# Kernel tuning notes

Hardware: AMD Instinct MI355X
Metric: run time of the kernel (lower is better)

The kernel has to match this reference:

```python
import jax, jax.numpy as jnp
from jax import lax
import numpy as np

D_MODEL = 128
N_HEADS = 8
N_POINTS = 8
MAX_MAG = 10.0
NEG_SLOPE = 0.1


def conv2d(x, w, b, pad):
    # x: (N, Cin, H, W), w: (Cout, Cin, kh, kw)
    y = lax.conv_general_dilated(x, w, (1, 1), [(pad, pad), (pad, pad)],
                                 dimension_numbers=('NCHW', 'OIHW', 'NCHW'))
    return y + b[None, :, None, None]


def leaky(x):
    return jnp.where(x >= 0, x, NEG_SLOPE * x)


def bilinear_sample(img, grid):
    # img: (B, C, H, W); grid: (B, P, H, W, 2) in [-1, 1] (x, y)
    # Matches torch F.grid_sample(mode='bilinear', padding_mode='zeros', align_corners=False)
    B, C, H, W = img.shape
    x = ((grid[..., 0] + 1.0) * W - 1.0) * 0.5
    y = ((grid[..., 1] + 1.0) * H - 1.0) * 0.5
    x0 = jnp.floor(x)
    y0 = jnp.floor(y)
    wx1 = x - x0
    wy1 = y - y0

    def one(img_b, x0b, y0b, wx1b, wy1b):
        def gather(xi, yi):
            valid = (xi >= 0) & (xi < W) & (yi >= 0) & (yi < H)
            xc = jnp.clip(xi, 0, W - 1).astype(jnp.int32)
            yc = jnp.clip(yi, 0, H - 1).astype(jnp.int32)
            v = img_b[:, yc, xc]  # (C, P, H, W)
            return v * valid
        wx0b = 1.0 - wx1b
        wy0b = 1.0 - wy1b
        v00 = gather(x0b, y0b)
        v01 = gather(x0b + 1, y0b)
        v10 = gather(x0b, y0b + 1)
        v11 = gather(x0b + 1, y0b + 1)
        return (v00 * (wx0b * wy0b) + v01 * (wx1b * wy0b)
                + v10 * (wx0b * wy1b) + v11 * (wx1b * wy1b))

    return jax.vmap(one)(img, x0, y0, wx1, wy1)  # (B, C, P, H, W)


def ss_deform_attn(value, loc):
    # value: (N, nh, d, H, W); loc: (N, nh, P, H, W, 2) in normalized [0,1] coords
    N, nh, d, H, W = value.shape
    P = loc.shape[2]
    v = value.reshape(N * nh, d, H, W)
    grids = (2.0 * loc - 1.0).reshape(N * nh, P, H, W, 2)
    sampled = bilinear_sample(v, grids)  # (N*nh, d, P, H, W)
    # per-location attention logits = <sampled_point, value_at_location>
    scores = jnp.einsum('ndphw,ndhw->nphw', sampled, v)
    aw = jax.nn.softmax(scores, axis=1)
    out = jnp.einsum('ndphw,nphw->ndhw', sampled, aw)
    return out.reshape(N, nh * d, H, W)


def _forward(query, value, reference_points, co_w1, co_b1, co_w2, co_b2,
             co_w3, co_b3, co_w4, co_b4, val_w, val_b, out_w, out_b):
    N, C, H, W = value.shape
    v = conv2d(value, val_w, val_b, 0)
    v = v.reshape(N, N_HEADS, D_MODEL // N_HEADS, H, W)
    o = leaky(conv2d(query, co_w1, co_b1, 1))
    o = leaky(conv2d(o, co_w2, co_b2, 1))
    o = leaky(conv2d(o, co_w3, co_b3, 1))
    o = conv2d(o, co_w4, co_b4, 1)
    o = MAX_MAG * jnp.tanh(o)
    offsets = o.reshape(N, N_HEADS, N_POINTS, H, W, 2)
    norm = jnp.array([W, H], dtype=o.dtype)  # (x, y) normalizer
    loc = reference_points[:, None, None, :, :, :] + offsets / norm
    out = ss_deform_attn(v, loc)
    return conv2d(out, out_w, out_b, 0)


def setup_inputs() -> dict:
    key = jax.random.key(0)
    ks = jax.random.split(key, 12)
    N, H, W = 4, 80, 80

    def w_init(k, shape):
        fan_in = shape[1] * shape[2] * shape[3]
        return jax.random.normal(k, shape, jnp.float32) / np.sqrt(fan_in)

    return {
        'query': jax.random.normal(ks[0], (N, 2 * D_MODEL, H, W), jnp.float32),
        'value': jax.random.normal(ks[1], (N, D_MODEL, H, W), jnp.float32),
        'reference_points': jax.random.uniform(ks[2], (N, H, W, 2), jnp.float32),
        'co_w1': w_init(ks[3], (D_MODEL, 2 * D_MODEL, 3, 3)),
        'co_b1': jnp.zeros((D_MODEL,), jnp.float32),
        'co_w2': w_init(ks[4], (D_MODEL, D_MODEL, 3, 3)),
        'co_b2': jnp.zeros((D_MODEL,), jnp.float32),
        'co_w3': w_init(ks[5], (D_MODEL, D_MODEL, 3, 3)),
        'co_b3': jnp.zeros((D_MODEL,), jnp.float32),
        'co_w4': w_init(ks[6], (N_HEADS * N_POINTS * 2, D_MODEL, 3, 3)),
        'co_b4': jnp.zeros((N_HEADS * N_POINTS * 2,), jnp.float32),
        'val_w': w_init(ks[7], (D_MODEL, D_MODEL, 1, 1)),
        'val_b': jnp.zeros((D_MODEL,), jnp.float32),
        'out_w': w_init(ks[8], (D_MODEL, D_MODEL, 1, 1)),
        'out_b': jnp.zeros((D_MODEL,), jnp.float32),
    }


def reference(query, value, reference_points, co_w1, co_b1, co_w2, co_b2,
              co_w3, co_b3, co_w4, co_b4, val_w, val_b, out_w, out_b):
    return _forward(query, value, reference_points, co_w1, co_b1, co_w2, co_b2,
                    co_w3, co_b3, co_w4, co_b4, val_w, val_b, out_w, out_b)
```

## Files before the change

kernel.cpp:

```cpp
#include <hip/hip_runtime.h>
#include <math.h>

#define Hh 80
#define Ww 80
#define HW 6400
#define PS 6724
#define NB 4

typedef _Float16 half8 __attribute__((ext_vector_type(8)));
typedef _Float16 half4v __attribute__((ext_vector_type(4)));
typedef float f32x16 __attribute__((ext_vector_type(16)));

__device__ __forceinline__ void gload16(const _Float16* g, _Float16* l) {
    __builtin_amdgcn_global_load_lds(
        (const __attribute__((address_space(1))) void*)g,
        (__attribute__((address_space(3))) void*)l, 16, 0, 0);
}

#define WAITVM(N) asm volatile("s_waitcnt vmcnt(" #N ")" ::: "memory")
#define FENCE() asm volatile("" ::: "memory")

__device__ __forceinline__ void barrier_mem() {
    asm volatile("" ::: "memory");
    __builtin_amdgcn_s_barrier();
    asm volatile("" ::: "memory");
}

__device__ inline void wblob_one(const float* src, _Float16* dst, int CI, int d) {
    int NC = CI / 32;
    int j = d & 7;
    int l = (d >> 3) & 63;
    int h = (d >> 9) & 1;
    int rest = d >> 10;
    int tap = rest % 9;
    rest /= 9;
    int c = rest % NC;
    int CT = rest / NC;
    int co = CT * 32 + (l & 31);
    int ci = c * 32 + h * 16 + (l >> 5) * 8 + j;
    dst[d] = (_Float16)src[((size_t)co * CI + ci) * 9 + tap];
}

__device__ inline void wblob1x1_one(const float* src, _Float16* dst, int d) {
    int j = d & 7;
    int l = (d >> 3) & 63;
    int c = (d >> 9) & 7;
    int CT = d >> 12;
    int co = CT * 32 + (l & 31);
    int ci = c * 16 + (l >> 5) * 8 + j;
    dst[d] = (_Float16)src[co * 128 + ci];
}

__device__ inline int padsite(int p) {
    if (p < 82) return p;
    if (p < 164) return 81 * 82 + (p - 82);
    if (p < 244) return (p - 163) * 82;
    return (p - 243) * 82 + 81;
}

__global__ __launch_bounds__(256) void prep_all(
    const float* __restrict__ w1, const float* __restrict__ w2,
    const float* __restrict__ w3, const float* __restrict__ w4,
    const float* __restrict__ vw, const float* __restrict__ ow,
    _Float16* __restrict__ b1, _Float16* __restrict__ b2,
    _Float16* __restrict__ b3, _Float16* __restrict__ b4,
    _Float16* __restrict__ bv, _Float16* __restrict__ bo,
    int* __restrict__ qh_i, int* __restrict__ hA_i, int* __restrict__ hB_i,
    const float* __restrict__ query, const float* __restrict__ value,
    _Float16* __restrict__ q_h, _Float16* __restrict__ v_h) {
    __shared__ _Float16 T[64 * 264];
    const int blk = blockIdx.x;
    const int t = threadIdx.x;

    if (blk < 4304) {
        int idx = blk * 256 + t;
        if (idx < 294912) { wblob_one(w1, b1, 256, idx); return; }
        idx -= 294912;
        if (idx < 147456) { wblob_one(w2, b2, 128, idx); return; }
        idx -= 147456;
        if (idx < 147456) { wblob_one(w3, b3, 128, idx); return; }
        idx -= 147456;
        if (idx < 147456) { wblob_one(w4, b4, 128, idx); return; }
        idx -= 147456;
        if (idx < 16384) { wblob1x1_one(vw, bv, idx); return; }
        idx -= 16384;
        if (idx < 16384) { wblob1x1_one(ow, bo, idx); return; }
        idx -= 16384;
        if (idx < 165888) {
            int n = idx / 41472, rr = idx % 41472;
            int c = rr / 5184, r2 = rr % 5184;
            int p = r2 >> 4, k = r2 & 15;
            qh_i[((size_t)(n * 8 + c) * PS + padsite(p)) * 16 + k] = 0;
            return;
        }
        idx -= 165888;
        if (idx < 82944) {
            int n = idx / 20736, rr = idx % 20736;
            int c = rr / 5184, r2 = rr % 5184;
            int p = r2 >> 4, k = r2 & 15;
            hA_i[((size_t)(n * 4 + c) * PS + padsite(p)) * 16 + k] = 0;
            return;
        }
        idx -= 82944;
        if (idx < 82944) {
            int n = idx / 20736, rr = idx % 20736;
            int c = rr / 5184, r2 = rr % 5184;
            int p = r2 >> 4, k = r2 & 15;
            hB_i[((size_t)(n * 4 + c) * PS + padsite(p)) * 16 + k] = 0;
        }
        return;
    }

    if (blk < 4704) {
        const int b = blk - 4304;
        const int xcd = b & 7, n = xcd & 3, hi = xcd >> 2;
        const int s0 = hi * 3200 + (b >> 3) * 64;
        constexpr int CI = 256, ST = CI + 8;
        for (int idx = t; idx < 64 * CI; idx += 256) {
            int ci = idx >> 6, sl = idx & 63;
            T[sl * ST + ci] = (_Float16)query[((size_t)n * CI + ci) * HW + s0 + sl];
        }
        __syncthreads();
        for (int idx = t; idx < 64 * 32; idx += 256) {
            int q = idx & 31, sl = idx >> 5;
            int s = s0 + sl, yy = s / 80, xx = s % 80;
            int c = q >> 2, off = (q & 3) * 8;
            *(int4*)(q_h + ((size_t)(n * 8 + c) * PS + (yy + 1) * 82 + (xx + 1)) * 32 + off) =
                *(const int4*)(&T[sl * ST + q * 8]);
        }
        return;
    }

    {
        const int b = blk - 4704;
        const int xcd = b & 7, n = xcd & 3, hi = xcd >> 2;
        const int s0 = hi * 3200 + (b >> 3) * 64;
        constexpr int CI = 128, ST = CI + 8;
        for (int idx = t; idx < 64 * CI; idx += 256) {
            int ci = idx >> 6, sl = idx & 63;
            T[sl * ST + ci] = (_Float16)value[((size_t)n * CI + ci) * HW + s0 + sl];
        }
        __syncthreads();
        for (int idx = t; idx < 64 * 16; idx += 256) {
            int q = idx & 15, sl = idx >> 4;
            *(int4*)(v_h + ((size_t)n * HW + s0 + sl) * CI + q * 8) =
                *(const int4*)(&T[sl * ST + q * 8]);
        }
    }
}

template <int NCp, int ACT>
__device__ __forceinline__ void conv3x3_body(
    int b, const _Float16* __restrict__ in, const _Float16* __restrict__ wblob,
    const float* __restrict__ bias, void* __restrict__ outp) {
    constexpr int NS = NCp * 18;
    static_assert((NCp & 1) == 0, "pair loop needs even NCp");
    __shared__ _Float16 Bbuf[2][6 * 1024];

    const int xcd = b & 7, n = xcd & 3, hi = xcd >> 2;
    const int r = b >> 3;
    const int x0 = (r % 5) * 16, y0 = hi * 40 + (r / 5) * 4;
    const int t = threadIdx.x;
    const int w = t >> 6, l = t & 63;
    const int lane31 = l & 31, lhalf = l >> 5;
    const int lx = lane31 & 15, lyw = lane31 >> 4;
    const int si = l & 15, g8 = l >> 4;

    const _Float16* bplane0 = in + (size_t)(n * NCp) * PS * 32;
    const _Float16* wA = wblob + (size_t)w * NS * 512 + l * 8;

    f32x16 acc0 = {}, acc1 = {};
    half8 aA[6], aB[6];

    auto stageB = [&](const _Float16* plane, int par) {
#pragma unroll
        for (int j = 0; j < 3; ++j) {
            const int m = 3 * w + j, rr = m >> 1, sg = m & 1;
            gload16(plane + ((size_t)((y0 + rr) * 82 + x0 + sg * 16 + si)) * 32 + g8 * 8,
                    &Bbuf[par][rr * 1024 + sg * 512]);
        }
    };
    auto loadA6 = [&](half8 (&ar)[6], int grp) {
        const _Float16* asrc = wA + (size_t)grp * 6 * 512;
#pragma unroll
        for (int k2 = 0; k2 < 6; ++k2)
            ar[k2] = *(const half8*)(asrc + (size_t)k2 * 512);
    };
    auto compute6 = [&](int gi, const half8 (&ar)[6], const _Float16* bb) {
#pragma unroll
        for (int k = 0; k < 6; ++k) {
            const int u = gi * 6 + k;
            const int tap = u >> 1, h = u & 1;
            const int dy = tap / 3, dx = tap % 3;
            const int cx = lx + dx;
            const int boff = (cx >> 4) * 512 + (h * 2 + lhalf) * 128 + (cx & 15) * 8;
            half8 b0 = *(const half8*)&bb[(lyw + dy) * 1024 + boff];
            half8 b1 = *(const half8*)&bb[(lyw + 2 + dy) * 1024 + boff];
            acc0 = __builtin_amdgcn_mfma_f32_32x32x16_f16(ar[k], b0, acc0, 0, 0, 0);
            acc1 = __builtin_amdgcn_mfma_f32_32x32x16_f16(ar[k], b1, acc1, 0, 0, 0);
        }
    };

    stageB(bplane0, 0);
    loadA6(aA, 0);
    WAITVM(0);
    barrier_mem();

#pragma unroll 1
    for (int cp = 0; cp < NCp / 2; ++cp) {
        const int c0 = 2 * cp;
        const bool lastp = (cp == NCp / 2 - 1);
        const _Float16* plane1 = bplane0 + (size_t)(c0 + 1) * PS * 32;
        const _Float16* plane2 = bplane0 + (size_t)(c0 + 2) * PS * 32;
        loadA6(aB, c0 * 3 + 1);
        stageB(plane1, 1);
        FENCE();
        compute6(0, aA, Bbuf[0]);
        loadA6(aA, c0 * 3 + 2);
        FENCE();
        compute6(1, aB, Bbuf[0]);
        loadA6(aB, c0 * 3 + 3);
        FENCE();
        compute6(2, aA, Bbuf[0]);
        WAITVM(12);
        barrier_mem();
        loadA6(aA, c0 * 3 + 4);
        if (!lastp) stageB(plane2, 0);
        FENCE();
        compute6(0, aB, Bbuf[1]);
        loadA6(aB, c0 * 3 + 5);
        FENCE();
        compute6(1, aA, Bbuf[1]);
        if (!lastp) {
            loadA6(aA, c0 * 3 + 6);
            FENCE();
            compute6(2, aB, Bbuf[1]);
            WAITVM(12);
            barrier_mem();
        } else {
            FENCE();
            compute6(2, aB, Bbuf[1]);
        }
    }

    const int x = x0 + lx;
#pragma unroll
    for (int f = 0; f < 2; ++f) {
        const f32x16& acc = f ? acc1 : acc0;
        const int y = y0 + lyw + 2 * f;
#pragma unroll
        for (int q = 0; q < 4; ++q) {
            const int inner = 8 * q + 4 * lhalf;
            const int co0 = w * 32 + inner;
            float v[4];
#pragma unroll
            for (int i = 0; i < 4; ++i) {
                float vv = acc[q * 4 + i] + bias[co0 + i];
                if (ACT == 1) vv = (vv >= 0.f) ? vv : 0.1f * vv;
                else vv = 10.f * tanhf(vv);
                v[i] = vv;
            }
            if (ACT == 1) {
                half4v hv = {(_Float16)v[0], (_Float16)v[1], (_Float16)v[2], (_Float16)v[3]};
                *(half4v*)((_Float16*)outp +
                    ((size_t)(n * 4 + w) * PS + (y + 1) * 82 + (x + 1)) * 32 + inner) = hv;
            } else {
                float4 fv = {v[0], v[1], v[2], v[3]};
                *(float4*)((float*)outp + ((size_t)n * HW + y * 80 + x) * 128 + co0) = fv;
            }
        }
    }
}

template <int NCp, int ACT>
__global__ __launch_bounds__(256, 2) void conv3x3_mfma(
    const _Float16* __restrict__ in, const _Float16* __restrict__ wblob,
    const float* __restrict__ bias, void* __restrict__ outp) {
    conv3x3_body<NCp, ACT>(blockIdx.x, in, wblob, bias, outp);
}

template <int MODE>
__device__ __forceinline__ void conv1x1_body(
    int b, const _Float16* __restrict__ in, const _Float16* __restrict__ wblob,
    const float* __restrict__ bias, float* __restrict__ outp) {
    const int xcd = b & 7, n = xcd & 3, hi = xcd >> 2;
    const int r = b >> 3;
    const int coH = r & 1, strip = r >> 1;
    const int t = threadIdx.x;
    const int w = t >> 6, l = t & 63;
    const int lane31 = l & 31, lhalf = l >> 5;
    const int s = hi * 3200 + strip * 128 + w * 32 + lane31;

    const _Float16* pB = in + (size_t)(n * HW + s) * 128 + lhalf * 8;
    const _Float16* pA0 = wblob + (size_t)(coH * 2) * 8 * 512 + l * 8;
    const _Float16* pA1 = pA0 + 8 * 512;

    half8 bB[8], bA0[8], bA1[8];
#pragma unroll
    for (int c = 0; c < 8; ++c) {
        bB[c]  = *(const half8*)(pB + c * 16);
        bA0[c] = *(const half8*)(pA0 + (size_t)c * 512);
        bA1[c] = *(const half8*)(pA1 + (size_t)c * 512);
    }
    f32x16 acc0 = {}, acc1 = {};
#pragma unroll
    for (int c = 0; c < 8; ++c) {
        acc0 = __builtin_amdgcn_mfma_f32_32x32x16_f16(bA0[c], bB[c], acc0, 0, 0, 0);
        acc1 = __builtin_amdgcn_mfma_f32_32x32x16_f16(bA1[c], bB[c], acc1, 0, 0, 0);
    }

#pragma unroll
    for (int ct = 0; ct < 2; ++ct) {
        const f32x16& acc = ct ? acc1 : acc0;
#pragma unroll
        for (int q = 0; q < 4; ++q) {
            const int co0 = coH * 64 + ct * 32 + 8 * q + 4 * lhalf;
            if (MODE == 0) {
                const int hd = co0 >> 4, dd = co0 & 15;
                float4 fv = {acc[4 * q + 0] + bias[co0 + 0], acc[4 * q + 1] + bias[co0 + 1],
                             acc[4 * q + 2] + bias[co0 + 2], acc[4 * q + 3] + bias[co0 + 3]};
                *(float4*)&outp[((size_t)(n * 8 + hd) * HW + s) * 16 + dd] = fv;
            } else {
#pragma unroll
                for (int i = 0; i < 4; ++i)
                    outp[(size_t)(n * 128 + co0 + i) * HW + s] = acc[4 * q + i] + bias[co0 + i];
            }
        }
    }
}

template <int MODE>
__global__ __launch_bounds__(256) void conv1x1_mfma(
    const _Float16* __restrict__ in, const _Float16* __restrict__ wblob,
    const float* __restrict__ bias, float* __restrict__ outp) {
    conv1x1_body<MODE>(blockIdx.x, in, wblob, bias, outp);
}

__global__ __launch_bounds__(256, 2) void conv1_val_fused(
    const _Float16* __restrict__ q_h, const _Float16* __restrict__ wb1,
    const float* __restrict__ co_b1, void* __restrict__ hA,
    const _Float16* __restrict__ v_h, const _Float16* __restrict__ wbv,
    const float* __restrict__ val_b, float* __restrict__ v_s) {
    const int b = blockIdx.x;
    if (b < 400) {
        conv3x3_body<8, 1>(b, q_h, wb1, co_b1, hA);
    } else {
        conv1x1_body<0>(b - 400, v_h, wbv, val_b, v_s);
    }
}

__global__ __launch_bounds__(256, 4) void deform_attn_kernel(
    const float* __restrict__ v_s, const float* __restrict__ offs,
    const float* __restrict__ ref, _Float16* __restrict__ att) {
    const int slice = blockIdx.x;
    const int n = slice >> 3, hd = slice & 7;
    const int t = threadIdx.x;
    const int s = blockIdx.y * 32 + (t >> 3);
    const int sub = t & 7;
    const int d0 = (sub & 3) * 4;
    const int ph = sub >> 2;
    const int nb = n * 8 + hd;
    const float* vbase = v_s + (size_t)nb * (HW * 16) + d0;

    const float4 cv = *(const float4*)&v_s[((size_t)nb * HW + s) * 16 + d0];
    const float rx = ref[(size_t)(n * HW + s) * 2 + 0] * 80.f - 0.5f;
    const float ry = ref[(size_t)(n * HW + s) * 2 + 1] * 80.f - 0.5f;

    const int e = (s >= 3200) ? 1 : 0;
    const float* ob0 = offs + ((size_t)n * HW + (2 * s - e * HW)) * 128 + hd * 16 + e;

    float4 oxv0 = *(const float4*)(ob0 + 8 * ph);
    float4 oxv1 = *(const float4*)(ob0 + 8 * ph + 4);
    float4 oyv0 = *(const float4*)(ob0 + 128 + 8 * ph);
    float4 oyv1 = *(const float4*)(ob0 + 128 + 8 * ph + 4);
    float ox[4] = {oxv0.x, oxv0.z, oxv1.x, oxv1.z};
    float oy[4] = {oyv0.x, oyv0.z, oyv1.x, oyv1.z};

    float wx1[4], wy1[4];
    int ix[4], iy[4];
#pragma unroll
    for (int p = 0; p < 4; ++p) {
        const float px = rx + ox[p];
        const float py = ry + oy[p];
        const float fx = floorf(px), fy = floorf(py);
        ix[p] = (int)fx; iy[p] = (int)fy;
        wx1[p] = px - fx; wy1[p] = py - fy;
    }

    float4 g[4][4];
#pragma unroll
    for (int p = 0; p < 4; ++p) {
        const int xc0 = min(max(ix[p], 0), 79),     xc1 = min(max(ix[p] + 1, 0), 79);
        const int yc0 = min(max(iy[p], 0), 79),     yc1 = min(max(iy[p] + 1, 0), 79);
        const int r0 = yc0 * 80, r1 = yc1 * 80;
        g[p][0] = *(const float4*)(vbase + (size_t)(r0 + xc0) * 16);
        g[p][1] = *(const float4*)(vbase + (size_t)(r0 + xc1) * 16);
        g[p][2] = *(const float4*)(vbase + (size_t)(r1 + xc0) * 16);
        g[p][3] = *(const float4*)(vbase + (size_t)(r1 + xc1) * 16);
    }

    float4 sampled[4];
    float score[4];
#pragma unroll
    for (int p = 0; p < 4; ++p) {
        const float vx0 = (ix[p] >= 0 && ix[p] < Ww) ? 1.f : 0.f;
        const float vx1 = (ix[p] + 1 >= 0 && ix[p] + 1 < Ww) ? 1.f : 0.f;
        const float vy0 = (iy[p] >= 0 && iy[p] < Hh) ? 1.f : 0.f;
        const float vy1 = (iy[p] + 1 >= 0 && iy[p] + 1 < Hh) ? 1.f : 0.f;
        const float wx0 = 1.f - wx1[p], wy0 = 1.f - wy1[p];
        const float w00 = wx0 * wy0 * vx0 * vy0;
        const float w01 = wx1[p] * wy0 * vx1 * vy0;
        const float w10 = wx0 * wy1[p] * vx0 * vy1;
        const float w11 = wx1[p] * wy1[p] * vx1 * vy1;
        float4 sv;
        sv.x = g[p][0].x * w00 + g[p][1].x * w01 + g[p][2].x * w10 + g[p][3].x * w11;
        sv.y = g[p][0].y * w00 + g[p][1].y * w01 + g[p][2].y * w10 + g[p][3].y * w11;
        sv.z = g[p][0].z * w00 + g[p][1].z * w01 + g[p][2].z * w10 + g[p][3].z * w11;
        sv.w = g[p][0].w * w00 + g[p][1].w * w01 + g[p][2].w * w10 + g[p][3].w * w11;
        sampled[p] = sv;
        float sc = sv.x * cv.x + sv.y * cv.y + sv.z * cv.z + sv.w * cv.w;
        sc += __shfl_xor(sc, 1);
        sc += __shfl_xor(sc, 2);
        score[p] = sc;
    }

    float m = score[0];
#pragma unroll
    for (int p = 1; p < 4; ++p) m = fmaxf(m, score[p]);
    float sum = 0.f;
    float4 o = {0.f, 0.f, 0.f, 0.f};
#pragma unroll
    for (int p = 0; p < 4; ++p) {
        const float aw = __expf(score[p] - m);
        sum += aw;
        o.x += aw * sampled[p].x;
        o.y += aw * sampled[p].y;
        o.z += aw * sampled[p].z;
        o.w += aw * sampled[p].w;
    }

    const float m2   = __shfl_xor(m, 4);
    const float sum2 = __shfl_xor(sum, 4);
    float4 o2;
    o2.x = __shfl_xor(o.x, 4);
    o2.y = __shfl_xor(o.y, 4);
    o2.z = __shfl_xor(o.z, 4);
    o2.w = __shfl_xor(o.w, 4);
    const float mn = fmaxf(m, m2);
    const float sA = __expf(m - mn), sB = __expf(m2 - mn);
    const float tot = sum * sA + sum2 * sB;
    const float inv = 1.f / tot;
    o.x = (o.x * sA + o2.x * sB) * inv;
    o.y = (o.y * sA + o2.y * sB) * inv;
    o.z = (o.z * sA + o2.z * sB) * inv;
    o.w = (o.w * sA + o2.w * sB) * inv;

    if (ph == 0) {
        half4v hv = {(_Float16)o.x, (_Float16)o.y, (_Float16)o.z, (_Float16)o.w};
        *(half4v*)&att[((size_t)n * HW + s) * 128 + hd * 16 + d0] = hv;
    }
}

extern "C" void kernel_launch(void* const* d_in, const int* in_sizes, int n_in,
                              void* d_out, int out_size, void* d_ws, size_t ws_size,
                              hipStream_t stream) {
    const float* query = (const float*)d_in[0];
    const float* value = (const float*)d_in[1];
    const float* ref   = (const float*)d_in[2];
    const float* co_w1 = (const float*)d_in[3];
    const float* co_b1 = (const float*)d_in[4];
    const float* co_w2 = (const float*)d_in[5];
    const float* co_b2 = (const float*)d_in[6];
    const float* co_w3 = (const float*)d_in[7];
    const float* co_b3 = (const float*)d_in[8];
    const float* co_w4 = (const float*)d_in[9];
    const float* co_b4 = (const float*)d_in[10];
    const float* val_w = (const float*)d_in[11];
    const float* val_b = (const float*)d_in[12];
    const float* out_w = (const float*)d_in[13];
    const float* out_b = (const float*)d_in[14];

    char* ws = (char*)d_ws;
    size_t o = 0;
    auto alloc = [&](size_t bytes) { char* p = ws + o; o += (bytes + 255) & ~(size_t)255; return p; };

    _Float16* wb1 = (_Float16*)alloc(294912 * 2);
    _Float16* wb2 = (_Float16*)alloc(147456 * 2);
    _Float16* wb3 = (_Float16*)alloc(147456 * 2);
    _Float16* wb4 = (_Float16*)alloc(147456 * 2);
    _Float16* wbv = (_Float16*)alloc(16384 * 2);
    _Float16* wbo = (_Float16*)alloc(16384 * 2);
    float* v_s = (float*)alloc(3276800 * 4);
    _Float16* v_h = (_Float16*)alloc((size_t)NB * HW * 128 * 2);
    char* R1 = alloc((size_t)NB * 8 * PS * 32 * 2);
    _Float16* q_h = (_Float16*)R1;
    float* o4 = (float*)R1;
    char* R2 = alloc((size_t)NB * 4 * PS * 32 * 2 * 2);
    _Float16* hA = (_Float16*)R2;
    _Float16* hB = (_Float16*)(R2 + (size_t)NB * 4 * PS * 32 * 2);
    _Float16* att_h = (_Float16*)R2;

    prep_all<<<5104, 256, 0, stream>>>(co_w1, co_w2, co_w3, co_w4, val_w, out_w,
                                       wb1, wb2, wb3, wb4, wbv, wbo,
                                       (int*)q_h, (int*)hA, (int*)hB,
                                       query, value, q_h, v_h);

    conv1_val_fused<<<800, 256, 0, stream>>>(q_h, wb1, co_b1, hA,
                                             v_h, wbv, val_b, v_s);

    conv3x3_mfma<4, 1><<<400, 256, 0, stream>>>(hA, wb2, co_b2, hB);
    conv3x3_mfma<4, 1><<<400, 256, 0, stream>>>(hB, wb3, co_b3, hA);
    conv3x3_mfma<4, 2><<<400, 256, 0, stream>>>(hA, wb4, co_b4, o4);

    deform_attn_kernel<<<dim3(32, 200), 256, 0, stream>>>(v_s, o4, ref, att_h);

    conv1x1_mfma<1><<<400, 256, 0, stream>>>(att_h, wbo, out_b, (float*)d_out);
}
```

Before: 217.6 us.

## Fuse deformable attention with output 1x1 projection via LDS staging

Merges the deformable attention kernel and the output 1x1 conv into one kernel. Each 1024-thread block computes all 8 heads for 16 sites, stages the fp16 attention result in shared memory, then 4 waves run MFMA to project to 128 output channels. This removes the global round-trip of the attention buffer and one kernel launch. The block-to-site mapping is also remapped so that neighbouring blocks share a batch image. In exchange, only a quarter of the threads do the projection, a block barrier is added, the output stores are strided by channel, and launch_bounds(1024,4) may constrain registers.

```diff
diff --git a/kernel.cpp b/kernel.cpp
--- a/kernel.cpp
+++ b/kernel.cpp
@@ -329,13 +329,6 @@
     }
 }
 
-template <int MODE>
-__global__ __launch_bounds__(256) void conv1x1_mfma(
-    const _Float16* __restrict__ in, const _Float16* __restrict__ wblob,
-    const float* __restrict__ bias, float* __restrict__ outp) {
-    conv1x1_body<MODE>(blockIdx.x, in, wblob, bias, outp);
-}
-
 __global__ __launch_bounds__(256, 2) void conv1_val_fused(
     const _Float16* __restrict__ q_h, const _Float16* __restrict__ wb1,
     const float* __restrict__ co_b1, void* __restrict__ hA,
@@ -349,14 +342,18 @@
     }
 }
 
-__global__ __launch_bounds__(256, 4) void deform_attn_kernel(
+__global__ __launch_bounds__(1024, 4) void deform_out_fused(
     const float* __restrict__ v_s, const float* __restrict__ offs,
-    const float* __restrict__ ref, _Float16* __restrict__ att) {
-    const int slice = blockIdx.x;
-    const int n = slice >> 3, hd = slice & 7;
+    const float* __restrict__ ref, const _Float16* __restrict__ wbo,
+    const float* __restrict__ out_b, float* __restrict__ outp) {
+    __shared__ _Float16 attT[16 * 136];
+    const int b = blockIdx.x;
+    const int xcd = b & 7, n = xcd & 3, hi = xcd >> 2;
+    const int g = b >> 3;
+    const int s0 = hi * 3200 + g * 16;
     const int t = threadIdx.x;
-    const int s = blockIdx.y * 32 + (t >> 3);
-    const int sub = t & 7;
+    const int sub = t & 7, hd = (t >> 3) & 7, sl = t >> 6;
+    const int s = s0 + sl;
     const int d0 = (sub & 3) * 4;
     const int ph = sub >> 2;
     const int nb = n * 8 + hd;
@@ -387,16 +384,16 @@
         wx1[p] = px - fx; wy1[p] = py - fy;
     }
 
-    float4 g[4][4];
+    float4 gg[4][4];
 #pragma unroll
     for (int p = 0; p < 4; ++p) {
         const int xc0 = min(max(ix[p], 0), 79),     xc1 = min(max(ix[p] + 1, 0), 79);
         const int yc0 = min(max(iy[p], 0), 79),     yc1 = min(max(iy[p] + 1, 0), 79);
         const int r0 = yc0 * 80, r1 = yc1 * 80;
-        g[p][0] = *(const float4*)(vbase + (size_t)(r0 + xc0) * 16);
-        g[p][1] = *(const float4*)(vbase + (size_t)(r0 + xc1) * 16);
-        g[p][2] = *(const float4*)(vbase + (size_t)(r1 + xc0) * 16);
-        g[p][3] = *(const float4*)(vbase + (size_t)(r1 + xc1) * 16);
+        gg[p][0] = *(const float4*)(vbase + (size_t)(r0 + xc0) * 16);
+        gg[p][1] = *(const float4*)(vbase + (size_t)(r0 + xc1) * 16);
+        gg[p][2] = *(const float4*)(vbase + (size_t)(r1 + xc0) * 16);
+        gg[p][3] = *(const float4*)(vbase + (size_t)(r1 + xc1) * 16);
     }
 
     float4 sampled[4];
@@ -413,10 +410,10 @@
         const float w10 = wx0 * wy1[p] * vx0 * vy1;
         const float w11 = wx1[p] * wy1[p] * vx1 * vy1;
         float4 sv;
-        sv.x = g[p][0].x * w00 + g[p][1].x * w01 + g[p][2].x * w10 + g[p][3].x * w11;
-        sv.y = g[p][0].y * w00 + g[p][1].y * w01 + g[p][2].y * w10 + g[p][3].y * w11;
-        sv.z = g[p][0].z * w00 + g[p][1].z * w01 + g[p][2].z * w10 + g[p][3].z * w11;
-        sv.w = g[p][0].w * w00 + g[p][1].w * w01 + g[p][2].w * w10 + g[p][3].w * w11;
+        sv.x = gg[p][0].x * w00 + gg[p][1].x * w01 + gg[p][2].x * w10 + gg[p][3].x * w11;
+        sv.y = gg[p][0].y * w00 + gg[p][1].y * w01 + gg[p][2].y * w10 + gg[p][3].y * w11;
+        sv.z = gg[p][0].z * w00 + gg[p][1].z * w01 + gg[p][2].z * w10 + gg[p][3].z * w11;
+        sv.w = gg[p][0].w * w00 + gg[p][1].w * w01 + gg[p][2].w * w10 + gg[p][3].w * w11;
         sampled[p] = sv;
         float sc = sv.x * cv.x + sv.y * cv.y + sv.z * cv.z + sv.w * cv.w;
         sc += __shfl_xor(sc, 1);
@@ -457,7 +454,35 @@
 
     if (ph == 0) {
         half4v hv = {(_Float16)o.x, (_Float16)o.y, (_Float16)o.z, (_Float16)o.w};
-        *(half4v*)&att[((size_t)n * HW + s) * 128 + hd * 16 + d0] = hv;
+        *(half4v*)&attT[sl * 136 + hd * 16 + d0] = hv;
+    }
+    __syncthreads();
+
+    if (t < 256) {
+        const int w = t >> 6, l = t & 63;
+        const int lane31 = l & 31, lhalf = l >> 5;
+        const int site = lane31 & 15;
+        const _Float16* pA = wbo + (size_t)w * 8 * 512 + l * 8;
+        half8 bB[8], bA[8];
+#pragma unroll
+        for (int c = 0; c < 8; ++c) {
+            bB[c] = *(const half8*)&attT[site * 136 + c * 16 + lhalf * 8];
+            bA[c] = *(const half8*)(pA + (size_t)c * 512);
+        }
+        f32x16 acc = {};
+#pragma unroll
+        for (int c = 0; c < 8; ++c)
+            acc = __builtin_amdgcn_mfma_f32_32x32x16_f16(bA[c], bB[c], acc, 0, 0, 0);
+        if (lane31 < 16) {
+#pragma unroll
+            for (int q = 0; q < 4; ++q) {
+                const int co0 = w * 32 + 8 * q + 4 * lhalf;
+#pragma unroll
+                for (int i = 0; i < 4; ++i)
+                    outp[(size_t)(n * 128 + co0 + i) * HW + s0 + site] =
+                        acc[4 * q + i] + out_b[co0 + i];
+            }
+        }
     }
 }
 
@@ -498,7 +523,6 @@
     char* R2 = alloc((size_t)NB * 4 * PS * 32 * 2 * 2);
     _Float16* hA = (_Float16*)R2;
     _Float16* hB = (_Float16*)(R2 + (size_t)NB * 4 * PS * 32 * 2);
-    _Float16* att_h = (_Float16*)R2;
 
     prep_all<<<5104, 256, 0, stream>>>(co_w1, co_w2, co_w3, co_w4, val_w, out_w,
                                        wb1, wb2, wb3, wb4, wbv, wbo,
@@ -512,7 +536,6 @@
     conv3x3_mfma<4, 1><<<400, 256, 0, stream>>>(hB, wb3, co_b3, hA);
     conv3x3_mfma<4, 2><<<400, 256, 0, stream>>>(hA, wb4, co_b4, o4);
 
-    deform_attn_kernel<<<dim3(32, 200), 256, 0, stream>>>(v_s, o4, ref, att_h);
-
-    conv1x1_mfma<1><<<400, 256, 0, stream>>>(att_h, wbo, out_b, (float*)d_out);
-}
+    deform_out_fused<<<1600, 1024, 0, stream>>>(v_s, o4, ref, wbo, out_b,
+                                                (float*)d_out);
+}
```

Result: no change. 216.7 us (-0.4%).
